# Kernel optimization log

Measured on AMD Instinct MI355X. Metric: run time of the kernel, lower is better.

Reference implementation:

```python
import jax, jax.numpy as jnp
import numpy as np

ALPHA = 100.0
EPS = 1e-12  # matches torch F.normalize eps


def l2norm(v, axis):
    n = jnp.linalg.norm(v, axis=axis, keepdims=True)
    return v / jnp.maximum(n, EPS)


def setup_inputs() -> dict:
    key = jax.random.key(0)
    k1, k2 = jax.random.split(key)
    x = jax.random.normal(k1, (32, 512, 32, 32), dtype=jnp.float32)
    vocabs = jax.random.uniform(k2, (64, 512), dtype=jnp.float32)  # torch.rand init
    return {"x": x, "vocabs": vocabs}


def reference(x, vocabs):
    # x: [N, C, H, W]; vocabs: [K, C]
    N, C, H, W = x.shape
    K = vocabs.shape[0]
    x = l2norm(x, axis=1)                       # normalize descriptors over C
    xf = x.reshape(N, C, H * W)                 # [N, C, P]

    # 1x1 conv with weight = 2*alpha*vocabs, bias = -alpha*||vocabs||
    w = 2.0 * ALPHA * vocabs                    # [K, C]
    b = -ALPHA * jnp.linalg.norm(vocabs, axis=1)  # [K]
    logits = jnp.einsum('ncp,kc->nkp', xf, w) + b[None, :, None]
    a = jax.nn.softmax(logits, axis=1)          # soft assignment over K

    # Distributive rewrite of sum_p a[n,k,p]*(x[n,c,p] - vocabs[k,c])
    vlad = jnp.einsum('nkp,ncp->nkc', a, xf) - a.sum(-1)[:, :, None] * vocabs[None]
    vlad = l2norm(vlad, axis=2)                 # intra-normalization
    vlad = vlad.reshape(N, K * C)
    return l2norm(vlad, axis=1)
```

## Files before the change

### kernel.cpp

```cpp
#include <hip/hip_runtime.h>
#include <math.h>
#include <stdint.h>

#define ALPHA 100.0f
#define EPSN 1e-12f

typedef __attribute__((ext_vector_type(8))) short bf16x8;
typedef __attribute__((ext_vector_type(16))) float f32x16;
typedef __attribute__((ext_vector_type(4))) unsigned int u32x4;

static __device__ __forceinline__ uint32_t f2bf(float f) {
    uint32_t u = __builtin_bit_cast(uint32_t, f);
    return (u + 0x7FFFu + ((u >> 16) & 1u)) >> 16;
}
static __device__ __forceinline__ float bfhi(uint32_t u) {
    return __builtin_bit_cast(float, u & 0xFFFF0000u);
}
static __device__ __forceinline__ float bflo(uint32_t u) {
    return __builtin_bit_cast(float, u << 16);
}
static __device__ __forceinline__ uint32_t stage1(float f) {
    uint32_t hi = f2bf(f);
    uint32_t lo = f2bf(f - __builtin_bit_cast(float, hi << 16));
    return (hi << 16) | lo;
}
static __device__ __forceinline__ uint32_t packbf(float a, float b) {
    return f2bf(a) | (f2bf(b) << 16);
}

__global__ __launch_bounds__(64) void prep_kernel(const float* __restrict__ v,
                                                  unsigned short* __restrict__ vh,
                                                  unsigned short* __restrict__ vl,
                                                  float* __restrict__ bias,
                                                  float* __restrict__ az) {
    int k = blockIdx.x, lane = threadIdx.x;
    az[k * 64 + lane] = 0.f;
    const float* row = v + k * 512;
    float ssq = 0.f;
#pragma unroll
    for (int i = 0; i < 8; ++i) {
        int c = lane + 64 * i;
        float f = row[c];
        ssq = fmaf(f, f, ssq);
        uint32_t hi = f2bf(f);
        uint32_t lo = f2bf(f - __builtin_bit_cast(float, hi << 16));
        vh[k * 512 + c] = (unsigned short)hi;
        vl[k * 512 + c] = (unsigned short)lo;
    }
#pragma unroll
    for (int off = 32; off > 0; off >>= 1) ssq += __shfl_xor(ssq, off, 64);
    if (lane == 0) bias[k] = -ALPHA * sqrtf(ssq);
}

__global__ __launch_bounds__(256) void assign_kernel(
    const float* __restrict__ x, const unsigned short* __restrict__ vh,
    const unsigned short* __restrict__ vl, const float* __restrict__ bias,
    unsigned short* __restrict__ aT, float* __restrict__ asum) {
    __shared__ uint32_t xs[32 * 66];
    __shared__ uint32_t vhs[64 * 18];
    __shared__ uint32_t vls[64 * 18];
    __shared__ float bias_l[64];
    __shared__ float xch[2][2][32];

    int tid = threadIdx.x, bx = blockIdx.x;
    int n = bx >> 4, pblk = (bx & 15) << 6;
    int l = tid & 63, w = tid >> 6;
    int kh = w & 1, ph = w >> 1;
    int h = l >> 5, cl = l & 31;

    if (tid < 64) bias_l[tid] = bias[tid];

    int xr = tid >> 4;
    int xq = (tid & 15) << 2;
    int vk = tid >> 2;
    int vj = (tid & 3) << 3;

    const float* xg = x + (size_t)n * 524288 + pblk;
    const unsigned short* vhg = vh + vk * 512 + vj;
    const unsigned short* vlg = vl + vk * 512 + vj;

    f32x16 acc;
#pragma unroll
    for (int r = 0; r < 16; ++r) acc[r] = 0.f;
    float ssq = 0.f;

    float4 pxa = *(const float4*)(xg + (size_t)xr * 1024 + xq);
    float4 pxb = *(const float4*)(xg + (size_t)(xr + 16) * 1024 + xq);
    u32x4 pvh = *(const u32x4*)vhg;
    u32x4 pvl = *(const u32x4*)vlg;

    for (int ch = 0; ch < 16; ++ch) {
        __syncthreads();
        *(uint2*)&xs[xr * 66 + xq] = make_uint2(stage1(pxa.x), stage1(pxa.y));
        *(uint2*)&xs[xr * 66 + xq + 2] = make_uint2(stage1(pxa.z), stage1(pxa.w));
        *(uint2*)&xs[(xr + 16) * 66 + xq] = make_uint2(stage1(pxb.x), stage1(pxb.y));
        *(uint2*)&xs[(xr + 16) * 66 + xq + 2] = make_uint2(stage1(pxb.z), stage1(pxb.w));
        int vb = vk * 18 + (vj >> 1);
        *(uint2*)&vhs[vb] = make_uint2(pvh[0], pvh[1]);
        *(uint2*)&vhs[vb + 2] = make_uint2(pvh[2], pvh[3]);
        *(uint2*)&vls[vb] = make_uint2(pvl[0], pvl[1]);
        *(uint2*)&vls[vb + 2] = make_uint2(pvl[2], pvl[3]);
        __syncthreads();
        if (ch < 15) {
            int c0 = (ch + 1) << 5;
            pxa = *(const float4*)(xg + (size_t)(c0 + xr) * 1024 + xq);
            pxb = *(const float4*)(xg + (size_t)(c0 + xr + 16) * 1024 + xq);
            pvh = *(const u32x4*)(vhg + c0);
            pvl = *(const u32x4*)(vlg + c0);
        }
#pragma unroll
        for (int s = 0; s < 2; ++s) {
            int va = (32 * kh + cl) * 18 + 8 * s + 4 * h;
            uint2 a0 = *(const uint2*)&vhs[va];
            uint2 a1 = *(const uint2*)&vhs[va + 2];
            uint2 b0 = *(const uint2*)&vls[va];
            uint2 b1 = *(const uint2*)&vls[va + 2];
            u32x4 ahp, alp;
            ahp[0] = a0.x; ahp[1] = a0.y; ahp[2] = a1.x; ahp[3] = a1.y;
            alp[0] = b0.x; alp[1] = b0.y; alp[2] = b1.x; alp[3] = b1.y;
            uint32_t wv[8];
#pragma unroll
            for (int j = 0; j < 8; ++j)
                wv[j] = xs[(16 * s + 8 * h + j) * 66 + 32 * ph + cl];
#pragma unroll
            for (int j = 0; j < 8; ++j) {
                float xv = bfhi(wv[j]) + bflo(wv[j]);
                ssq = fmaf(xv, xv, ssq);
            }
            u32x4 bhp, blp;
#pragma unroll
            for (int q = 0; q < 4; ++q) {
                bhp[q] = (wv[2 * q] >> 16) | (wv[2 * q + 1] & 0xFFFF0000u);
                blp[q] = (wv[2 * q] & 0xFFFFu) | (wv[2 * q + 1] << 16);
            }
            bf16x8 ah = __builtin_bit_cast(bf16x8, ahp);
            bf16x8 al = __builtin_bit_cast(bf16x8, alp);
            bf16x8 bh = __builtin_bit_cast(bf16x8, bhp);
            bf16x8 bl = __builtin_bit_cast(bf16x8, blp);
            acc = __builtin_amdgcn_mfma_f32_32x32x16_bf16(ah, bh, acc, 0, 0, 0);
            acc = __builtin_amdgcn_mfma_f32_32x32x16_bf16(ah, bl, acc, 0, 0, 0);
            acc = __builtin_amdgcn_mfma_f32_32x32x16_bf16(al, bh, acc, 0, 0, 0);
        }
    }
    ssq += __shfl_xor(ssq, 32, 64);
    float sinv = 1.0f / fmaxf(sqrtf(ssq), EPSN);
    float twoAs = 2.0f * ALPHA * sinv;
    float e[16];
    float m = -INFINITY;
#pragma unroll
    for (int r = 0; r < 16; ++r) {
        int k = (r & 3) + 8 * (r >> 2) + 4 * h + 32 * kh;
        float lv = fmaf(twoAs, acc[r], bias_l[k]);
        e[r] = lv;
        m = fmaxf(m, lv);
    }
    m = fmaxf(m, __shfl_xor(m, 32, 64));
    __syncthreads();
    if (l < 32) xch[kh][ph][l] = m;
    __syncthreads();
    m = fmaxf(m, xch[1 - kh][ph][cl]);
    float ssum = 0.f;
#pragma unroll
    for (int r = 0; r < 16; ++r) {
        e[r] = expf(e[r] - m);
        ssum += e[r];
    }
    ssum += __shfl_xor(ssum, 32, 64);
    __syncthreads();
    if (l < 32) xch[kh][ph][l] = ssum;
    __syncthreads();
    ssum += xch[1 - kh][ph][cl];
    float rs = 1.0f / ssum;
    float a2s = rs * sinv;
    unsigned short* aTn = aT + (size_t)n * 65536 + pblk + 32 * ph + cl;
#pragma unroll
    for (int r = 0; r < 16; ++r) {
        int k = (r & 3) + 8 * (r >> 2) + 4 * h + 32 * kh;
        aTn[(size_t)k * 1024] = (unsigned short)f2bf(e[r] * a2s);
        float red = e[r] * rs;
#pragma unroll
        for (int off = 1; off <= 16; off <<= 1) red += __shfl_xor(red, off, 64);
        if (cl == 0) atomicAdd(&asum[n * 64 + k], red);
    }
}

__global__ __launch_bounds__(256) void vlad_kernel(
    const float* __restrict__ x, const unsigned short* __restrict__ aT,
    const float* __restrict__ asum, const float* __restrict__ vocabs,
    float* __restrict__ out, float* __restrict__ knorm) {
    __shared__ uint32_t xt[32 * 34];
    __shared__ uint32_t at[64 * 34];
    __shared__ float cmb[2][64][16];
    __shared__ float asum_l[64];

    int tid = threadIdx.x, bx = blockIdx.x;
    int n = bx >> 4, cb = (bx & 15) << 5;
    int l = tid & 63, w = tid >> 6;
    int kh = w & 1, ps = w >> 1;
    int h = l >> 5, cl = l & 31;

    if (tid < 64) asum_l[tid] = asum[n * 64 + tid];

    int xr = tid >> 3;
    int xq = (tid & 7) << 2;
    int ak = tid >> 2;
    int aj = (tid & 3) << 4;

    const float* xg = x + (size_t)n * 524288 + (size_t)(cb + xr) * 1024 + xq;
    const unsigned short* ag = aT + (size_t)n * 65536 + (size_t)ak * 1024 + aj;

    f32x16 acc;
#pragma unroll
    for (int r = 0; r < 16; ++r) acc[r] = 0.f;

    float4 pxa = *(const float4*)xg;
    float4 pxb = *(const float4*)(xg + 32);
    u32x4 pa0 = *(const u32x4*)ag;
    u32x4 pa1 = *(const u32x4*)(ag + 8);

    for (int ch = 0; ch < 16; ++ch) {
        __syncthreads();
        int xb = xr * 34 + (xq >> 1);
        *(uint2*)&xt[xb] = make_uint2(packbf(pxa.x, pxa.y), packbf(pxa.z, pxa.w));
        *(uint2*)&xt[xb + 16] = make_uint2(packbf(pxb.x, pxb.y), packbf(pxb.z, pxb.w));
        int ab = ak * 34 + (aj >> 1);
        *(uint2*)&at[ab] = make_uint2(pa0[0], pa0[1]);
        *(uint2*)&at[ab + 2] = make_uint2(pa0[2], pa0[3]);
        *(uint2*)&at[ab + 4] = make_uint2(pa1[0], pa1[1]);
        *(uint2*)&at[ab + 6] = make_uint2(pa1[2], pa1[3]);
        __syncthreads();
        if (ch < 15) {
            int p0 = (ch + 1) << 6;
            pxa = *(const float4*)(xg + p0);
            pxb = *(const float4*)(xg + p0 + 32);
            pa0 = *(const u32x4*)(ag + p0);
            pa1 = *(const u32x4*)(ag + p0 + 8);
        }
        if (ps == (ch & 1)) {
#pragma unroll
            for (int s = 0; s < 4; ++s) {
                int va = (32 * kh + cl) * 34 + 8 * s + 4 * h;
                uint2 f0 = *(const uint2*)&at[va];
                uint2 f1 = *(const uint2*)&at[va + 2];
                int vb = cl * 34 + 8 * s + 4 * h;
                uint2 g0 = *(const uint2*)&xt[vb];
                uint2 g1 = *(const uint2*)&xt[vb + 2];
                u32x4 afp, bfp;
                afp[0] = f0.x; afp[1] = f0.y; afp[2] = f1.x; afp[3] = f1.y;
                bfp[0] = g0.x; bfp[1] = g0.y; bfp[2] = g1.x; bfp[3] = g1.y;
                acc = __builtin_amdgcn_mfma_f32_32x32x16_bf16(
                    __builtin_bit_cast(bf16x8, afp),
                    __builtin_bit_cast(bf16x8, bfp), acc, 0, 0, 0);
            }
        }
    }
    __syncthreads();
    if (ps == 1) {
#pragma unroll
        for (int r = 0; r < 16; ++r) cmb[kh][l][r] = acc[r];
    }
    __syncthreads();
    if (ps == 0) {
#pragma unroll
        for (int r = 0; r < 16; ++r) {
            int k = (r & 3) + 8 * (r >> 2) + 4 * h + 32 * kh;
            int c = cb + cl;
            float val = acc[r] + cmb[kh][l][r];
            val = fmaf(-asum_l[k], vocabs[k * 512 + c], val);
            out[(size_t)n * 32768 + (size_t)k * 512 + c] = val;
            float t2 = val * val;
#pragma unroll
            for (int off = 1; off <= 16; off <<= 1) t2 += __shfl_xor(t2, off, 64);
            if (cl == 0) atomicAdd(&knorm[n * 64 + k], t2);
        }
    }
}

__global__ __launch_bounds__(256) void scale_kernel(float* __restrict__ out,
                                                    const float* __restrict__ knorm) {
    int n = blockIdx.y;
    int sb = blockIdx.x;
    int tid = threadIdx.x;
    __shared__ float sc[64];
    __shared__ float tots;
    if (tid < 64) {
        float kn = knorm[n * 64 + tid];
        float nk = sqrtf(kn);
        float inv = 1.0f / fmaxf(nk, EPSN);
        sc[tid] = inv;
        float t = nk * inv;
        float t2 = t * t;
#pragma unroll
        for (int off = 32; off > 0; off >>= 1) t2 += __shfl_xor(t2, off, 64);
        if (tid == 0) tots = t2;
    }
    __syncthreads();
    float invt = 1.0f / fmaxf(sqrtf(tots), EPSN);
    float* base = out + (size_t)n * 32768 + sb * 4096;
#pragma unroll
    for (int i = 0; i < 16; ++i) {
        int idx = tid + 256 * i;
        int k = (sb * 4096 + idx) >> 9;
        base[idx] *= sc[k] * invt;
    }
}

extern "C" void kernel_launch(void* const* d_in, const int* in_sizes, int n_in,
                              void* d_out, int out_size, void* d_ws, size_t ws_size,
                              hipStream_t stream) {
    const float* x = (const float*)d_in[0];
    const float* vocabs = (const float*)d_in[1];
    float* out = (float*)d_out;
    char* ws = (char*)d_ws;
    unsigned short* vh = (unsigned short*)(ws);
    unsigned short* vl = (unsigned short*)(ws + 65536);
    float* bias  = (float*)(ws + 131072);
    float* asum  = (float*)(ws + 131328);
    float* knorm = (float*)(ws + 139520);
    unsigned short* aT = (unsigned short*)(ws + 147712);

    prep_kernel<<<64, 64, 0, stream>>>(vocabs, vh, vl, bias, asum);
    assign_kernel<<<512, 256, 0, stream>>>(x, vh, vl, bias, aT, asum);
    vlad_kernel<<<512, 256, 0, stream>>>(x, aT, asum, vocabs, out, knorm);
    scale_kernel<<<dim3(8, 32), 256, 0, stream>>>(out, knorm);
}
```

Before: 139.7 us.

## Fuse soft-assignment and VLAD aggregation into one kernel using atomic accumulation

The assignment and aggregation kernels are merged into one. Each block keeps its 32-pixel x tile resident in LDS as bf16, computes the softmax assignment, then multiplies the assignment by x with 16x16x32 MFMAs and adds partial results into the zeroed output with float atomics. The global round trip of the assignment matrix and the second read of x go away. In exchange there is a memset, a separate correction kernel for the -asum*vocab term and the norms, and a very large number of global float atomics (1024 blocks each adding into the full 64x512 slice) that may serialize.

Result: slower. 218.5 us (+56.4%).

```diff
diff --git a/kernel.cpp b/kernel.cpp
--- a/kernel.cpp
+++ b/kernel.cpp
@@ -6,26 +6,15 @@
 #define EPSN 1e-12f
 
 typedef __attribute__((ext_vector_type(8))) short bf16x8;
-typedef __attribute__((ext_vector_type(16))) float f32x16;
+typedef __attribute__((ext_vector_type(4))) float f32x4;
 typedef __attribute__((ext_vector_type(4))) unsigned int u32x4;
 
 static __device__ __forceinline__ uint32_t f2bf(float f) {
     uint32_t u = __builtin_bit_cast(uint32_t, f);
     return (u + 0x7FFFu + ((u >> 16) & 1u)) >> 16;
 }
-static __device__ __forceinline__ float bfhi(uint32_t u) {
-    return __builtin_bit_cast(float, u & 0xFFFF0000u);
-}
-static __device__ __forceinline__ float bflo(uint32_t u) {
-    return __builtin_bit_cast(float, u << 16);
-}
-static __device__ __forceinline__ uint32_t stage1(float f) {
-    uint32_t hi = f2bf(f);
-    uint32_t lo = f2bf(f - __builtin_bit_cast(float, hi << 16));
-    return (hi << 16) | lo;
-}
-static __device__ __forceinline__ uint32_t packbf(float a, float b) {
-    return f2bf(a) | (f2bf(b) << 16);
+static __device__ __forceinline__ float bf2f(uint32_t b) {
+    return __builtin_bit_cast(float, b << 16);
 }
 
 __global__ __launch_bounds__(64) void prep_kernel(const float* __restrict__ v,
@@ -43,7 +32,7 @@
         float f = row[c];
         ssq = fmaf(f, f, ssq);
         uint32_t hi = f2bf(f);
-        uint32_t lo = f2bf(f - __builtin_bit_cast(float, hi << 16));
+        uint32_t lo = f2bf(f - bf2f(hi));
         vh[k * 512 + c] = (unsigned short)hi;
         vl[k * 512 + c] = (unsigned short)lo;
     }
@@ -52,50 +41,59 @@
     if (lane == 0) bias[k] = -ALPHA * sqrtf(ssq);
 }
 
-__global__ __launch_bounds__(256) void assign_kernel(
+__global__ __launch_bounds__(256) void fused_kernel(
     const float* __restrict__ x, const unsigned short* __restrict__ vh,
     const unsigned short* __restrict__ vl, const float* __restrict__ bias,
-    unsigned short* __restrict__ aT, float* __restrict__ asum) {
-    __shared__ uint32_t xs[32 * 66];
-    __shared__ uint32_t vhs[64 * 18];
-    __shared__ uint32_t vls[64 * 18];
+    float* __restrict__ out, float* __restrict__ asum) {
+    __shared__ uint32_t xs2[512 * 20];
+    __shared__ uint32_t xsp[32 * 34];
+    __shared__ uint32_t vhs[64 * 20];
+    __shared__ uint32_t vls[64 * 20];
+    __shared__ float Lbuf[64 * 34];
+    __shared__ unsigned short a2s[64 * 40];
+    __shared__ float sinv_s[32];
     __shared__ float bias_l[64];
-    __shared__ float xch[2][2][32];
+    __shared__ float ssqx[4][8][4];
+    __shared__ float xch[32][8];
 
     int tid = threadIdx.x, bx = blockIdx.x;
-    int n = bx >> 4, pblk = (bx & 15) << 6;
+    int n = bx & 31, pblk = (bx >> 5) << 5;
     int l = tid & 63, w = tid >> 6;
-    int kh = w & 1, ph = w >> 1;
-    int h = l >> 5, cl = l & 31;
+    int kb = w << 4;
+    int quad = l >> 4, m = l & 15;
 
     if (tid < 64) bias_l[tid] = bias[tid];
 
-    int xr = tid >> 4;
-    int xq = (tid & 15) << 2;
-    int vk = tid >> 2;
-    int vj = (tid & 3) << 3;
+    int sc = tid >> 3;
+    int sp4 = (tid & 7) << 2;
+    int vk = tid >> 2, vj = (tid & 3) << 3;
 
     const float* xg = x + (size_t)n * 524288 + pblk;
     const unsigned short* vhg = vh + vk * 512 + vj;
     const unsigned short* vlg = vl + vk * 512 + vj;
 
-    f32x16 acc;
-#pragma unroll
-    for (int r = 0; r < 16; ++r) acc[r] = 0.f;
-    float ssq = 0.f;
-
-    float4 pxa = *(const float4*)(xg + (size_t)xr * 1024 + xq);
-    float4 pxb = *(const float4*)(xg + (size_t)(xr + 16) * 1024 + xq);
+    f32x4 acc0, acc1;
+#pragma unroll
+    for (int r = 0; r < 4; ++r) { acc0[r] = 0.f; acc1[r] = 0.f; }
+    float sq0 = 0.f, sq1 = 0.f, sq2 = 0.f, sq3 = 0.f;
+
+    float4 px = *(const float4*)(xg + (size_t)sc * 1024 + sp4);
     u32x4 pvh = *(const u32x4*)vhg;
     u32x4 pvl = *(const u32x4*)vlg;
 
     for (int ch = 0; ch < 16; ++ch) {
         __syncthreads();
-        *(uint2*)&xs[xr * 66 + xq] = make_uint2(stage1(pxa.x), stage1(pxa.y));
-        *(uint2*)&xs[xr * 66 + xq + 2] = make_uint2(stage1(pxa.z), stage1(pxa.w));
-        *(uint2*)&xs[(xr + 16) * 66 + xq] = make_uint2(stage1(pxb.x), stage1(pxb.y));
-        *(uint2*)&xs[(xr + 16) * 66 + xq + 2] = make_uint2(stage1(pxb.z), stage1(pxb.w));
-        int vb = vk * 18 + (vj >> 1);
+        float4 v4 = px;
+        sq0 = fmaf(v4.x, v4.x, sq0); sq1 = fmaf(v4.y, v4.y, sq1);
+        sq2 = fmaf(v4.z, v4.z, sq2); sq3 = fmaf(v4.w, v4.w, sq3);
+        uint32_t h0 = f2bf(v4.x), h1 = f2bf(v4.y), h2 = f2bf(v4.z), h3 = f2bf(v4.w);
+        uint32_t lo0 = f2bf(v4.x - bf2f(h0)), lo1 = f2bf(v4.y - bf2f(h1));
+        uint32_t lo2 = f2bf(v4.z - bf2f(h2)), lo3 = f2bf(v4.w - bf2f(h3));
+        *(uint2*)&xsp[sc * 34 + sp4] = make_uint2((h0 << 16) | lo0, (h1 << 16) | lo1);
+        *(uint2*)&xsp[sc * 34 + sp4 + 2] = make_uint2((h2 << 16) | lo2, (h3 << 16) | lo3);
+        *(uint2*)&xs2[(ch * 32 + sc) * 20 + (sp4 >> 1)] =
+            make_uint2(h0 | (h1 << 16), h2 | (h3 << 16));
+        int vb = vk * 20 + (vj >> 1);
         *(uint2*)&vhs[vb] = make_uint2(pvh[0], pvh[1]);
         *(uint2*)&vhs[vb + 2] = make_uint2(pvh[2], pvh[3]);
         *(uint2*)&vls[vb] = make_uint2(pvl[0], pvl[1]);
@@ -103,177 +101,137 @@
         __syncthreads();
         if (ch < 15) {
             int c0 = (ch + 1) << 5;
-            pxa = *(const float4*)(xg + (size_t)(c0 + xr) * 1024 + xq);
-            pxb = *(const float4*)(xg + (size_t)(c0 + xr + 16) * 1024 + xq);
+            px = *(const float4*)(xg + (size_t)(c0 + sc) * 1024 + sp4);
             pvh = *(const u32x4*)(vhg + c0);
             pvl = *(const u32x4*)(vlg + c0);
         }
-#pragma unroll
-        for (int s = 0; s < 2; ++s) {
-            int va = (32 * kh + cl) * 18 + 8 * s + 4 * h;
-            uint2 a0 = *(const uint2*)&vhs[va];
-            uint2 a1 = *(const uint2*)&vhs[va + 2];
-            uint2 b0 = *(const uint2*)&vls[va];
-            uint2 b1 = *(const uint2*)&vls[va + 2];
-            u32x4 ahp, alp;
-            ahp[0] = a0.x; ahp[1] = a0.y; ahp[2] = a1.x; ahp[3] = a1.y;
-            alp[0] = b0.x; alp[1] = b0.y; alp[2] = b1.x; alp[3] = b1.y;
+        int va = (kb + m) * 20 + (quad << 2);
+        bf16x8 ah = *(const bf16x8*)&vhs[va];
+        bf16x8 al = *(const bf16x8*)&vls[va];
+#pragma unroll
+        for (int f = 0; f < 2; ++f) {
+            int p = (f << 4) + m;
             uint32_t wv[8];
 #pragma unroll
-            for (int j = 0; j < 8; ++j)
-                wv[j] = xs[(16 * s + 8 * h + j) * 66 + 32 * ph + cl];
-#pragma unroll
-            for (int j = 0; j < 8; ++j) {
-                float xv = bfhi(wv[j]) + bflo(wv[j]);
-                ssq = fmaf(xv, xv, ssq);
-            }
+            for (int j = 0; j < 8; ++j) wv[j] = xsp[(quad * 8 + j) * 34 + p];
             u32x4 bhp, blp;
 #pragma unroll
             for (int q = 0; q < 4; ++q) {
                 bhp[q] = (wv[2 * q] >> 16) | (wv[2 * q + 1] & 0xFFFF0000u);
                 blp[q] = (wv[2 * q] & 0xFFFFu) | (wv[2 * q + 1] << 16);
             }
-            bf16x8 ah = __builtin_bit_cast(bf16x8, ahp);
-            bf16x8 al = __builtin_bit_cast(bf16x8, alp);
             bf16x8 bh = __builtin_bit_cast(bf16x8, bhp);
             bf16x8 bl = __builtin_bit_cast(bf16x8, blp);
-            acc = __builtin_amdgcn_mfma_f32_32x32x16_bf16(ah, bh, acc, 0, 0, 0);
-            acc = __builtin_amdgcn_mfma_f32_32x32x16_bf16(ah, bl, acc, 0, 0, 0);
-            acc = __builtin_amdgcn_mfma_f32_32x32x16_bf16(al, bh, acc, 0, 0, 0);
-        }
-    }
-    ssq += __shfl_xor(ssq, 32, 64);
-    float sinv = 1.0f / fmaxf(sqrtf(ssq), EPSN);
-    float twoAs = 2.0f * ALPHA * sinv;
-    float e[16];
-    float m = -INFINITY;
-#pragma unroll
-    for (int r = 0; r < 16; ++r) {
-        int k = (r & 3) + 8 * (r >> 2) + 4 * h + 32 * kh;
-        float lv = fmaf(twoAs, acc[r], bias_l[k]);
-        e[r] = lv;
-        m = fmaxf(m, lv);
-    }
-    m = fmaxf(m, __shfl_xor(m, 32, 64));
-    __syncthreads();
-    if (l < 32) xch[kh][ph][l] = m;
-    __syncthreads();
-    m = fmaxf(m, xch[1 - kh][ph][cl]);
-    float ssum = 0.f;
-#pragma unroll
-    for (int r = 0; r < 16; ++r) {
-        e[r] = expf(e[r] - m);
-        ssum += e[r];
-    }
-    ssum += __shfl_xor(ssum, 32, 64);
-    __syncthreads();
-    if (l < 32) xch[kh][ph][l] = ssum;
-    __syncthreads();
-    ssum += xch[1 - kh][ph][cl];
-    float rs = 1.0f / ssum;
-    float a2s = rs * sinv;
-    unsigned short* aTn = aT + (size_t)n * 65536 + pblk + 32 * ph + cl;
-#pragma unroll
-    for (int r = 0; r < 16; ++r) {
-        int k = (r & 3) + 8 * (r >> 2) + 4 * h + 32 * kh;
-        aTn[(size_t)k * 1024] = (unsigned short)f2bf(e[r] * a2s);
-        float red = e[r] * rs;
-#pragma unroll
-        for (int off = 1; off <= 16; off <<= 1) red += __shfl_xor(red, off, 64);
-        if (cl == 0) atomicAdd(&asum[n * 64 + k], red);
-    }
-}
-
-__global__ __launch_bounds__(256) void vlad_kernel(
-    const float* __restrict__ x, const unsigned short* __restrict__ aT,
-    const float* __restrict__ asum, const float* __restrict__ vocabs,
-    float* __restrict__ out, float* __restrict__ knorm) {
-    __shared__ uint32_t xt[32 * 34];
-    __shared__ uint32_t at[64 * 34];
-    __shared__ float cmb[2][64][16];
-    __shared__ float asum_l[64];
-
-    int tid = threadIdx.x, bx = blockIdx.x;
-    int n = bx >> 4, cb = (bx & 15) << 5;
-    int l = tid & 63, w = tid >> 6;
-    int kh = w & 1, ps = w >> 1;
-    int h = l >> 5, cl = l & 31;
-
-    if (tid < 64) asum_l[tid] = asum[n * 64 + tid];
-
-    int xr = tid >> 3;
-    int xq = (tid & 7) << 2;
-    int ak = tid >> 2;
-    int aj = (tid & 3) << 4;
-
-    const float* xg = x + (size_t)n * 524288 + (size_t)(cb + xr) * 1024 + xq;
-    const unsigned short* ag = aT + (size_t)n * 65536 + (size_t)ak * 1024 + aj;
-
-    f32x16 acc;
-#pragma unroll
-    for (int r = 0; r < 16; ++r) acc[r] = 0.f;
-
-    float4 pxa = *(const float4*)xg;
-    float4 pxb = *(const float4*)(xg + 32);
-    u32x4 pa0 = *(const u32x4*)ag;
-    u32x4 pa1 = *(const u32x4*)(ag + 8);
-
-    for (int ch = 0; ch < 16; ++ch) {
-        __syncthreads();
-        int xb = xr * 34 + (xq >> 1);
-        *(uint2*)&xt[xb] = make_uint2(packbf(pxa.x, pxa.y), packbf(pxa.z, pxa.w));
-        *(uint2*)&xt[xb + 16] = make_uint2(packbf(pxb.x, pxb.y), packbf(pxb.z, pxb.w));
-        int ab = ak * 34 + (aj >> 1);
-        *(uint2*)&at[ab] = make_uint2(pa0[0], pa0[1]);
-        *(uint2*)&at[ab + 2] = make_uint2(pa0[2], pa0[3]);
-        *(uint2*)&at[ab + 4] = make_uint2(pa1[0], pa1[1]);
-        *(uint2*)&at[ab + 6] = make_uint2(pa1[2], pa1[3]);
-        __syncthreads();
-        if (ch < 15) {
-            int p0 = (ch + 1) << 6;
-            pxa = *(const float4*)(xg + p0);
-            pxb = *(const float4*)(xg + p0 + 32);
-            pa0 = *(const u32x4*)(ag + p0);
-            pa1 = *(const u32x4*)(ag + p0 + 8);
-        }
-        if (ps == (ch & 1)) {
-#pragma unroll
-            for (int s = 0; s < 4; ++s) {
-                int va = (32 * kh + cl) * 34 + 8 * s + 4 * h;
-                uint2 f0 = *(const uint2*)&at[va];
-                uint2 f1 = *(const uint2*)&at[va + 2];
-                int vb = cl * 34 + 8 * s + 4 * h;
-                uint2 g0 = *(const uint2*)&xt[vb];
-                uint2 g1 = *(const uint2*)&xt[vb + 2];
-                u32x4 afp, bfp;
-                afp[0] = f0.x; afp[1] = f0.y; afp[2] = f1.x; afp[3] = f1.y;
-                bfp[0] = g0.x; bfp[1] = g0.y; bfp[2] = g1.x; bfp[3] = g1.y;
-                acc = __builtin_amdgcn_mfma_f32_32x32x16_bf16(
-                    __builtin_bit_cast(bf16x8, afp),
-                    __builtin_bit_cast(bf16x8, bfp), acc, 0, 0, 0);
+            if (f == 0) {
+                acc0 = __builtin_amdgcn_mfma_f32_16x16x32_bf16(ah, bh, acc0, 0, 0, 0);
+                acc0 = __builtin_amdgcn_mfma_f32_16x16x32_bf16(ah, bl, acc0, 0, 0, 0);
+                acc0 = __builtin_amdgcn_mfma_f32_16x16x32_bf16(al, bh, acc0, 0, 0, 0);
+            } else {
+                acc1 = __builtin_amdgcn_mfma_f32_16x16x32_bf16(ah, bh, acc1, 0, 0, 0);
+                acc1 = __builtin_amdgcn_mfma_f32_16x16x32_bf16(ah, bl, acc1, 0, 0, 0);
+                acc1 = __builtin_amdgcn_mfma_f32_16x16x32_bf16(al, bh, acc1, 0, 0, 0);
             }
         }
     }
-    __syncthreads();
-    if (ps == 1) {
-#pragma unroll
-        for (int r = 0; r < 16; ++r) cmb[kh][l][r] = acc[r];
-    }
-    __syncthreads();
-    if (ps == 0) {
-#pragma unroll
-        for (int r = 0; r < 16; ++r) {
-            int k = (r & 3) + 8 * (r >> 2) + 4 * h + 32 * kh;
-            int c = cb + cl;
-            float val = acc[r] + cmb[kh][l][r];
-            val = fmaf(-asum_l[k], vocabs[k * 512 + c], val);
-            out[(size_t)n * 32768 + (size_t)k * 512 + c] = val;
-            float t2 = val * val;
-#pragma unroll
-            for (int off = 1; off <= 16; off <<= 1) t2 += __shfl_xor(t2, off, 64);
-            if (cl == 0) atomicAdd(&knorm[n * 64 + k], t2);
-        }
-    }
+#pragma unroll
+    for (int mask = 8; mask <= 32; mask <<= 1) {
+        sq0 += __shfl_xor(sq0, mask, 64); sq1 += __shfl_xor(sq1, mask, 64);
+        sq2 += __shfl_xor(sq2, mask, 64); sq3 += __shfl_xor(sq3, mask, 64);
+    }
+    if (l < 8) {
+        ssqx[w][l][0] = sq0; ssqx[w][l][1] = sq1;
+        ssqx[w][l][2] = sq2; ssqx[w][l][3] = sq3;
+    }
+#pragma unroll
+    for (int r = 0; r < 4; ++r) {
+        Lbuf[(kb + quad * 4 + r) * 34 + m] = acc0[r];
+        Lbuf[(kb + quad * 4 + r) * 34 + 16 + m] = acc1[r];
+    }
+    __syncthreads();
+    if (tid < 32) {
+        int pq = tid >> 2, cm = tid & 3;
+        float s = ssqx[0][pq][cm] + ssqx[1][pq][cm] + ssqx[2][pq][cm] + ssqx[3][pq][cm];
+        sinv_s[tid] = 1.0f / fmaxf(sqrtf(s), EPSN);
+    }
+    __syncthreads();
+    int p = tid & 31, seg = tid >> 5;
+    float sv = sinv_s[p];
+    float tA = 2.0f * ALPHA * sv;
+    float d[8];
+    float mx = -INFINITY;
+#pragma unroll
+    for (int j = 0; j < 8; ++j) {
+        d[j] = fmaf(tA, Lbuf[(seg * 8 + j) * 34 + p], bias_l[seg * 8 + j]);
+        mx = fmaxf(mx, d[j]);
+    }
+    xch[p][seg] = mx;
+    __syncthreads();
+#pragma unroll
+    for (int q = 0; q < 8; ++q) mx = fmaxf(mx, xch[p][q]);
+    float s = 0.f;
+#pragma unroll
+    for (int j = 0; j < 8; ++j) {
+        d[j] = expf(d[j] - mx);
+        s += d[j];
+    }
+    __syncthreads();
+    xch[p][seg] = s;
+    __syncthreads();
+    s = 0.f;
+#pragma unroll
+    for (int q = 0; q < 8; ++q) s += xch[p][q];
+    float rs = 1.0f / s;
+    float a2f = rs * sv;
+#pragma unroll
+    for (int j = 0; j < 8; ++j) {
+        a2s[(seg * 8 + j) * 40 + p] = (unsigned short)f2bf(d[j] * a2f);
+        float red = d[j] * rs;
+#pragma unroll
+        for (int off = 1; off <= 16; off <<= 1) red += __shfl_xor(red, off, 64);
+        if ((l & 31) == 0) atomicAdd(&asum[n * 64 + seg * 8 + j], red);
+    }
+    __syncthreads();
+    bf16x8 afr = *(const bf16x8*)&a2s[(kb + m) * 40 + (quad << 3)];
+    f32x4 zero4;
+#pragma unroll
+    for (int r = 0; r < 4; ++r) zero4[r] = 0.f;
+    float* outb = out + (size_t)n * 32768 + (size_t)(kb + (quad << 2)) * 512;
+#pragma unroll 4
+    for (int cc = 0; cc < 32; ++cc) {
+        int cr = (cc << 4) + m;
+        u32x4 bp = *(const u32x4*)&xs2[cr * 20 + (quad << 2)];
+        f32x4 dres = __builtin_amdgcn_mfma_f32_16x16x32_bf16(
+            afr, __builtin_bit_cast(bf16x8, bp), zero4, 0, 0, 0);
+        float* po = outb + cr;
+        atomicAdd(po, dres[0]);
+        atomicAdd(po + 512, dres[1]);
+        atomicAdd(po + 1024, dres[2]);
+        atomicAdd(po + 1536, dres[3]);
+    }
+}
+
+__global__ __launch_bounds__(64) void correct_kernel(
+    float* __restrict__ out, const float* __restrict__ v,
+    const float* __restrict__ asum, float* __restrict__ knorm) {
+    int k = blockIdx.x, n = blockIdx.y, l = threadIdx.x;
+    float as = asum[n * 64 + k];
+    float* base = out + (size_t)n * 32768 + (size_t)k * 512;
+    const float* vr = v + k * 512;
+    float4 o0 = ((float4*)base)[l];
+    float4 o1 = ((float4*)base)[l + 64];
+    float4 v0 = ((const float4*)vr)[l];
+    float4 v1 = ((const float4*)vr)[l + 64];
+    o0.x = fmaf(-as, v0.x, o0.x); o0.y = fmaf(-as, v0.y, o0.y);
+    o0.z = fmaf(-as, v0.z, o0.z); o0.w = fmaf(-as, v0.w, o0.w);
+    o1.x = fmaf(-as, v1.x, o1.x); o1.y = fmaf(-as, v1.y, o1.y);
+    o1.z = fmaf(-as, v1.z, o1.z); o1.w = fmaf(-as, v1.w, o1.w);
+    ((float4*)base)[l] = o0;
+    ((float4*)base)[l + 64] = o1;
+    float ssq = o0.x * o0.x + o0.y * o0.y + o0.z * o0.z + o0.w * o0.w +
+                o1.x * o1.x + o1.y * o1.y + o1.z * o1.z + o1.w * o1.w;
+#pragma unroll
+    for (int off = 32; off > 0; off >>= 1) ssq += __shfl_xor(ssq, off, 64);
+    if (l == 0) knorm[n * 64 + k] = ssq;
 }
 
 __global__ __launch_bounds__(256) void scale_kernel(float* __restrict__ out,
@@ -317,10 +275,10 @@
     float* bias  = (float*)(ws + 131072);
     float* asum  = (float*)(ws + 131328);
     float* knorm = (float*)(ws + 139520);
-    unsigned short* aT = (unsigned short*)(ws + 147712);
-
+
+    hipMemsetAsync(out, 0, (size_t)32 * 32768 * 4, stream);
     prep_kernel<<<64, 64, 0, stream>>>(vocabs, vh, vl, bias, asum);
-    assign_kernel<<<512, 256, 0, stream>>>(x, vh, vl, bias, aT, asum);
-    vlad_kernel<<<512, 256, 0, stream>>>(x, aT, asum, vocabs, out, knorm);
+    fused_kernel<<<1024, 256, 0, stream>>>(x, vh, vl, bias, out, asum);
+    correct_kernel<<<dim3(64, 32), 64, 0, stream>>>(out, vocabs, asum, knorm);
     scale_kernel<<<dim3(8, 32), 256, 0, stream>>>(out, knorm);
 }
```

## Double-buffer LDS tiles in assign and vlad kernels with one barrier per stage

Applied to the files above, without the earlier changes.

Both the assign and VLAD GEMM kernels now use two LDS buffers and a two-deep register prefetch. Staging the next chunk overlaps with MFMA compute on the current one, so each chunk needs one barrier instead of two. A custom barrier that waits on lgkmcnt(0) and then issues s_barrier replaces __syncthreads, and the loop is fully unrolled. In exchange, LDS use and register pressure roughly double, which can lower occupancy.

New measurement: 137.0 us. Within noise of the previous version (-1.9%).

```diff
diff --git a/kernel.cpp b/kernel.cpp
--- a/kernel.cpp
+++ b/kernel.cpp
@@ -26,6 +26,9 @@
 }
 static __device__ __forceinline__ uint32_t packbf(float a, float b) {
     return f2bf(a) | (f2bf(b) << 16);
+}
+static __device__ __forceinline__ void lds_barrier() {
+    asm volatile("s_waitcnt lgkmcnt(0)\n\ts_barrier" ::: "memory");
 }
 
 __global__ __launch_bounds__(64) void prep_kernel(const float* __restrict__ v,
@@ -52,13 +55,79 @@
     if (lane == 0) bias[k] = -ALPHA * sqrtf(ssq);
 }
 
+static __device__ __forceinline__ void a_load(float4& pxa, float4& pxb,
+                                              u32x4& pvh, u32x4& pvl,
+                                              const float* xg,
+                                              const unsigned short* vhg,
+                                              const unsigned short* vlg,
+                                              int c0, int xr, int xq) {
+    pxa = *(const float4*)(xg + (size_t)(c0 + xr) * 1024 + xq);
+    pxb = *(const float4*)(xg + (size_t)(c0 + xr + 16) * 1024 + xq);
+    pvh = *(const u32x4*)(vhg + c0);
+    pvl = *(const u32x4*)(vlg + c0);
+}
+static __device__ __forceinline__ void a_stage(uint32_t* xsb, uint32_t* vhsb,
+                                               uint32_t* vlsb, const float4 pxa,
+                                               const float4 pxb, const u32x4 pvh,
+                                               const u32x4 pvl, int xr, int xq,
+                                               int vk, int vj) {
+    *(uint2*)&xsb[xr * 66 + xq] = make_uint2(stage1(pxa.x), stage1(pxa.y));
+    *(uint2*)&xsb[xr * 66 + xq + 2] = make_uint2(stage1(pxa.z), stage1(pxa.w));
+    *(uint2*)&xsb[(xr + 16) * 66 + xq] = make_uint2(stage1(pxb.x), stage1(pxb.y));
+    *(uint2*)&xsb[(xr + 16) * 66 + xq + 2] = make_uint2(stage1(pxb.z), stage1(pxb.w));
+    int vb = vk * 18 + (vj >> 1);
+    *(uint2*)&vhsb[vb] = make_uint2(pvh[0], pvh[1]);
+    *(uint2*)&vhsb[vb + 2] = make_uint2(pvh[2], pvh[3]);
+    *(uint2*)&vlsb[vb] = make_uint2(pvl[0], pvl[1]);
+    *(uint2*)&vlsb[vb + 2] = make_uint2(pvl[2], pvl[3]);
+}
+static __device__ __forceinline__ void a_compute(const uint32_t* xsb,
+                                                 const uint32_t* vhsb,
+                                                 const uint32_t* vlsb,
+                                                 f32x16& acc, float& ssq,
+                                                 int kh, int ph, int h, int cl) {
+#pragma unroll
+    for (int s = 0; s < 2; ++s) {
+        int va = (32 * kh + cl) * 18 + 8 * s + 4 * h;
+        uint2 a0 = *(const uint2*)&vhsb[va];
+        uint2 a1 = *(const uint2*)&vhsb[va + 2];
+        uint2 b0 = *(const uint2*)&vlsb[va];
+        uint2 b1 = *(const uint2*)&vlsb[va + 2];
+        u32x4 ahp, alp;
+        ahp[0] = a0.x; ahp[1] = a0.y; ahp[2] = a1.x; ahp[3] = a1.y;
+        alp[0] = b0.x; alp[1] = b0.y; alp[2] = b1.x; alp[3] = b1.y;
+        uint32_t wv[8];
+#pragma unroll
+        for (int j = 0; j < 8; ++j)
+            wv[j] = xsb[(16 * s + 8 * h + j) * 66 + 32 * ph + cl];
+#pragma unroll
+        for (int j = 0; j < 8; ++j) {
+            float xv = bfhi(wv[j]) + bflo(wv[j]);
+            ssq = fmaf(xv, xv, ssq);
+        }
+        u32x4 bhp, blp;
+#pragma unroll
+        for (int q = 0; q < 4; ++q) {
+            bhp[q] = (wv[2 * q] >> 16) | (wv[2 * q + 1] & 0xFFFF0000u);
+            blp[q] = (wv[2 * q] & 0xFFFFu) | (wv[2 * q + 1] << 16);
+        }
+        bf16x8 ah = __builtin_bit_cast(bf16x8, ahp);
+        bf16x8 al = __builtin_bit_cast(bf16x8, alp);
+        bf16x8 bh = __builtin_bit_cast(bf16x8, bhp);
+        bf16x8 bl = __builtin_bit_cast(bf16x8, blp);
+        acc = __builtin_amdgcn_mfma_f32_32x32x16_bf16(ah, bh, acc, 0, 0, 0);
+        acc = __builtin_amdgcn_mfma_f32_32x32x16_bf16(ah, bl, acc, 0, 0, 0);
+        acc = __builtin_amdgcn_mfma_f32_32x32x16_bf16(al, bh, acc, 0, 0, 0);
+    }
+}
+
 __global__ __launch_bounds__(256) void assign_kernel(
     const float* __restrict__ x, const unsigned short* __restrict__ vh,
     const unsigned short* __restrict__ vl, const float* __restrict__ bias,
     unsigned short* __restrict__ aT, float* __restrict__ asum) {
-    __shared__ uint32_t xs[32 * 66];
-    __shared__ uint32_t vhs[64 * 18];
-    __shared__ uint32_t vls[64 * 18];
+    __shared__ uint32_t xs[2][32 * 66];
+    __shared__ uint32_t vhs[2][64 * 18];
+    __shared__ uint32_t vls[2][64 * 18];
     __shared__ float bias_l[64];
     __shared__ float xch[2][2][32];
 
@@ -70,10 +139,8 @@
 
     if (tid < 64) bias_l[tid] = bias[tid];
 
-    int xr = tid >> 4;
-    int xq = (tid & 15) << 2;
-    int vk = tid >> 2;
-    int vj = (tid & 3) << 3;
+    int xr = tid >> 4, xq = (tid & 15) << 2;
+    int vk = tid >> 2, vj = (tid & 3) << 3;
 
     const float* xg = x + (size_t)n * 524288 + pblk;
     const unsigned short* vhg = vh + vk * 512 + vj;
@@ -84,63 +151,26 @@
     for (int r = 0; r < 16; ++r) acc[r] = 0.f;
     float ssq = 0.f;
 
-    float4 pxa = *(const float4*)(xg + (size_t)xr * 1024 + xq);
-    float4 pxb = *(const float4*)(xg + (size_t)(xr + 16) * 1024 + xq);
-    u32x4 pvh = *(const u32x4*)vhg;
-    u32x4 pvl = *(const u32x4*)vlg;
-
-    for (int ch = 0; ch < 16; ++ch) {
-        __syncthreads();
-        *(uint2*)&xs[xr * 66 + xq] = make_uint2(stage1(pxa.x), stage1(pxa.y));
-        *(uint2*)&xs[xr * 66 + xq + 2] = make_uint2(stage1(pxa.z), stage1(pxa.w));
-        *(uint2*)&xs[(xr + 16) * 66 + xq] = make_uint2(stage1(pxb.x), stage1(pxb.y));
-        *(uint2*)&xs[(xr + 16) * 66 + xq + 2] = make_uint2(stage1(pxb.z), stage1(pxb.w));
-        int vb = vk * 18 + (vj >> 1);
-        *(uint2*)&vhs[vb] = make_uint2(pvh[0], pvh[1]);
-        *(uint2*)&vhs[vb + 2] = make_uint2(pvh[2], pvh[3]);
-        *(uint2*)&vls[vb] = make_uint2(pvl[0], pvl[1]);
-        *(uint2*)&vls[vb + 2] = make_uint2(pvl[2], pvl[3]);
-        __syncthreads();
-        if (ch < 15) {
-            int c0 = (ch + 1) << 5;
-            pxa = *(const float4*)(xg + (size_t)(c0 + xr) * 1024 + xq);
-            pxb = *(const float4*)(xg + (size_t)(c0 + xr + 16) * 1024 + xq);
-            pvh = *(const u32x4*)(vhg + c0);
-            pvl = *(const u32x4*)(vlg + c0);
-        }
-#pragma unroll
-        for (int s = 0; s < 2; ++s) {
-            int va = (32 * kh + cl) * 18 + 8 * s + 4 * h;
-            uint2 a0 = *(const uint2*)&vhs[va];
-            uint2 a1 = *(const uint2*)&vhs[va + 2];
-            uint2 b0 = *(const uint2*)&vls[va];
-            uint2 b1 = *(const uint2*)&vls[va + 2];
-            u32x4 ahp, alp;
-            ahp[0] = a0.x; ahp[1] = a0.y; ahp[2] = a1.x; ahp[3] = a1.y;
-            alp[0] = b0.x; alp[1] = b0.y; alp[2] = b1.x; alp[3] = b1.y;
-            uint32_t wv[8];
-#pragma unroll
-            for (int j = 0; j < 8; ++j)
-                wv[j] = xs[(16 * s + 8 * h + j) * 66 + 32 * ph + cl];
-#pragma unroll
-            for (int j = 0; j < 8; ++j) {
-                float xv = bfhi(wv[j]) + bflo(wv[j]);
-                ssq = fmaf(xv, xv, ssq);
-            }
-            u32x4 bhp, blp;
-#pragma unroll
-            for (int q = 0; q < 4; ++q) {
-                bhp[q] = (wv[2 * q] >> 16) | (wv[2 * q + 1] & 0xFFFF0000u);
-                blp[q] = (wv[2 * q] & 0xFFFFu) | (wv[2 * q + 1] << 16);
-            }
-            bf16x8 ah = __builtin_bit_cast(bf16x8, ahp);
-            bf16x8 al = __builtin_bit_cast(bf16x8, alp);
-            bf16x8 bh = __builtin_bit_cast(bf16x8, bhp);
-            bf16x8 bl = __builtin_bit_cast(bf16x8, blp);
-            acc = __builtin_amdgcn_mfma_f32_32x32x16_bf16(ah, bh, acc, 0, 0, 0);
-            acc = __builtin_amdgcn_mfma_f32_32x32x16_bf16(ah, bl, acc, 0, 0, 0);
-            acc = __builtin_amdgcn_mfma_f32_32x32x16_bf16(al, bh, acc, 0, 0, 0);
-        }
+    float4 pxa[2], pxb[2];
+    u32x4 pvh[2], pvl[2];
+    a_load(pxa[0], pxb[0], pvh[0], pvl[0], xg, vhg, vlg, 0, xr, xq);
+    a_load(pxa[1], pxb[1], pvh[1], pvl[1], xg, vhg, vlg, 32, xr, xq);
+    __syncthreads();
+    a_stage(xs[0], vhs[0], vls[0], pxa[0], pxb[0], pvh[0], pvl[0], xr, xq, vk, vj);
+    lds_barrier();
+#pragma unroll
+    for (int cc = 0; cc < 8; ++cc) {
+        a_stage(xs[1], vhs[1], vls[1], pxa[1], pxb[1], pvh[1], pvl[1], xr, xq, vk, vj);
+        if (cc < 7)
+            a_load(pxa[0], pxb[0], pvh[0], pvl[0], xg, vhg, vlg, (2 * cc + 2) << 5, xr, xq);
+        a_compute(xs[0], vhs[0], vls[0], acc, ssq, kh, ph, h, cl);
+        lds_barrier();
+        if (cc < 7) {
+            a_stage(xs[0], vhs[0], vls[0], pxa[0], pxb[0], pvh[0], pvl[0], xr, xq, vk, vj);
+            a_load(pxa[1], pxb[1], pvh[1], pvl[1], xg, vhg, vlg, (2 * cc + 3) << 5, xr, xq);
+        }
+        a_compute(xs[1], vhs[1], vls[1], acc, ssq, kh, ph, h, cl);
+        lds_barrier();
     }
     ssq += __shfl_xor(ssq, 32, 64);
     float sinv = 1.0f / fmaxf(sqrtf(ssq), EPSN);
@@ -184,12 +214,55 @@
     }
 }
 
+static __device__ __forceinline__ void v_load(float4& qxa, float4& qxb,
+                                              u32x4& qa0, u32x4& qa1,
+                                              const float* xg,
+                                              const unsigned short* ag, int p0) {
+    qxa = *(const float4*)(xg + p0);
+    qxb = *(const float4*)(xg + p0 + 32);
+    qa0 = *(const u32x4*)(ag + p0);
+    qa1 = *(const u32x4*)(ag + p0 + 8);
+}
+static __device__ __forceinline__ void v_stage(uint32_t* xtb, uint32_t* atb,
+                                               const float4 qxa, const float4 qxb,
+                                               const u32x4 qa0, const u32x4 qa1,
+                                               int xr, int xq, int ak, int aj) {
+    int xb = xr * 34 + (xq >> 1);
+    *(uint2*)&xtb[xb] = make_uint2(packbf(qxa.x, qxa.y), packbf(qxa.z, qxa.w));
+    *(uint2*)&xtb[xb + 16] = make_uint2(packbf(qxb.x, qxb.y), packbf(qxb.z, qxb.w));
+    int ab = ak * 34 + (aj >> 1);
+    *(uint2*)&atb[ab] = make_uint2(qa0[0], qa0[1]);
+    *(uint2*)&atb[ab + 2] = make_uint2(qa0[2], qa0[3]);
+    *(uint2*)&atb[ab + 4] = make_uint2(qa1[0], qa1[1]);
+    *(uint2*)&atb[ab + 6] = make_uint2(qa1[2], qa1[3]);
+}
+static __device__ __forceinline__ void v_compute(const uint32_t* xtb,
+                                                 const uint32_t* atb,
+                                                 f32x16& acc, int kh, int h,
+                                                 int cl) {
+#pragma unroll
+    for (int s = 0; s < 4; ++s) {
+        int va = (32 * kh + cl) * 34 + 8 * s + 4 * h;
+        uint2 f0 = *(const uint2*)&atb[va];
+        uint2 f1 = *(const uint2*)&atb[va + 2];
+        int vb = cl * 34 + 8 * s + 4 * h;
+        uint2 g0 = *(const uint2*)&xtb[vb];
+        uint2 g1 = *(const uint2*)&xtb[vb + 2];
+        u32x4 afp, bfp;
+        afp[0] = f0.x; afp[1] = f0.y; afp[2] = f1.x; afp[3] = f1.y;
+        bfp[0] = g0.x; bfp[1] = g0.y; bfp[2] = g1.x; bfp[3] = g1.y;
+        acc = __builtin_amdgcn_mfma_f32_32x32x16_bf16(
+            __builtin_bit_cast(bf16x8, afp), __builtin_bit_cast(bf16x8, bfp),
+            acc, 0, 0, 0);
+    }
+}
+
 __global__ __launch_bounds__(256) void vlad_kernel(
     const float* __restrict__ x, const unsigned short* __restrict__ aT,
     const float* __restrict__ asum, const float* __restrict__ vocabs,
     float* __restrict__ out, float* __restrict__ knorm) {
-    __shared__ uint32_t xt[32 * 34];
-    __shared__ uint32_t at[64 * 34];
+    __shared__ uint32_t xt[2][32 * 34];
+    __shared__ uint32_t at[2][64 * 34];
     __shared__ float cmb[2][64][16];
     __shared__ float asum_l[64];
 
@@ -201,10 +274,8 @@
 
     if (tid < 64) asum_l[tid] = asum[n * 64 + tid];
 
-    int xr = tid >> 3;
-    int xq = (tid & 7) << 2;
-    int ak = tid >> 2;
-    int aj = (tid & 3) << 4;
+    int xr = tid >> 3, xq = (tid & 7) << 2;
+    int ak = tid >> 2, aj = (tid & 3) << 4;
 
     const float* xg = x + (size_t)n * 524288 + (size_t)(cb + xr) * 1024 + xq;
     const unsigned short* ag = aT + (size_t)n * 65536 + (size_t)ak * 1024 + aj;
@@ -213,46 +284,26 @@
 #pragma unroll
     for (int r = 0; r < 16; ++r) acc[r] = 0.f;
 
-    float4 pxa = *(const float4*)xg;
-    float4 pxb = *(const float4*)(xg + 32);
-    u32x4 pa0 = *(const u32x4*)ag;
-    u32x4 pa1 = *(const u32x4*)(ag + 8);
-
-    for (int ch = 0; ch < 16; ++ch) {
-        __syncthreads();
-        int xb = xr * 34 + (xq >> 1);
-        *(uint2*)&xt[xb] = make_uint2(packbf(pxa.x, pxa.y), packbf(pxa.z, pxa.w));
-        *(uint2*)&xt[xb + 16] = make_uint2(packbf(pxb.x, pxb.y), packbf(pxb.z, pxb.w));
-        int ab = ak * 34 + (aj >> 1);
-        *(uint2*)&at[ab] = make_uint2(pa0[0], pa0[1]);
-        *(uint2*)&at[ab + 2] = make_uint2(pa0[2], pa0[3]);
-        *(uint2*)&at[ab + 4] = make_uint2(pa1[0], pa1[1]);
-        *(uint2*)&at[ab + 6] = make_uint2(pa1[2], pa1[3]);
-        __syncthreads();
-        if (ch < 15) {
-            int p0 = (ch + 1) << 6;
-            pxa = *(const float4*)(xg + p0);
-            pxb = *(const float4*)(xg + p0 + 32);
-            pa0 = *(const u32x4*)(ag + p0);
-            pa1 = *(const u32x4*)(ag + p0 + 8);
-        }
-        if (ps == (ch & 1)) {
-#pragma unroll
-            for (int s = 0; s < 4; ++s) {
-                int va = (32 * kh + cl) * 34 + 8 * s + 4 * h;
-                uint2 f0 = *(const uint2*)&at[va];
-                uint2 f1 = *(const uint2*)&at[va + 2];
-                int vb = cl * 34 + 8 * s + 4 * h;
-                uint2 g0 = *(const uint2*)&xt[vb];
-                uint2 g1 = *(const uint2*)&xt[vb + 2];
-                u32x4 afp, bfp;
-                afp[0] = f0.x; afp[1] = f0.y; afp[2] = f1.x; afp[3] = f1.y;
-                bfp[0] = g0.x; bfp[1] = g0.y; bfp[2] = g1.x; bfp[3] = g1.y;
-                acc = __builtin_amdgcn_mfma_f32_32x32x16_bf16(
-                    __builtin_bit_cast(bf16x8, afp),
-                    __builtin_bit_cast(bf16x8, bfp), acc, 0, 0, 0);
-            }
-        }
+    float4 qxa[2], qxb[2];
+    u32x4 qa0[2], qa1[2];
+    v_load(qxa[0], qxb[0], qa0[0], qa1[0], xg, ag, 0);
+    v_load(qxa[1], qxb[1], qa0[1], qa1[1], xg, ag, 64);
+    __syncthreads();
+    v_stage(xt[0], at[0], qxa[0], qxb[0], qa0[0], qa1[0], xr, xq, ak, aj);
+    lds_barrier();
+#pragma unroll
+    for (int cc = 0; cc < 8; ++cc) {
+        v_stage(xt[1], at[1], qxa[1], qxb[1], qa0[1], qa1[1], xr, xq, ak, aj);
+        if (cc < 7)
+            v_load(qxa[0], qxb[0], qa0[0], qa1[0], xg, ag, (2 * cc + 2) << 6);
+        if (ps == 0) v_compute(xt[0], at[0], acc, kh, h, cl);
+        lds_barrier();
+        if (cc < 7) {
+            v_stage(xt[0], at[0], qxa[0], qxb[0], qa0[0], qa1[0], xr, xq, ak, aj);
+            v_load(qxa[1], qxb[1], qa0[1], qa1[1], xg, ag, (2 * cc + 3) << 6);
+        }
+        if (ps == 1) v_compute(xt[1], at[1], acc, kh, h, cl);
+        lds_barrier();
     }
     __syncthreads();
     if (ps == 1) {
```
